# Optimization experiments

Hardware: AMD Instinct MI355X
Metric: run time of the kernel (lower is better)

The kernel has to match this reference:

```python
import jax, jax.numpy as jnp
import numpy as np

B, N, DIM = 4, 2048, 64  # batch, seq_len (== gate out dim), model dim (== dim_head)
H, DH = 8, 64            # heads, dim_head


def setup_inputs() -> dict:
    key = jax.random.key(0)
    ks = jax.random.split(key, 12)
    inner = H * DH
    inp = {
        'q': jax.random.normal(ks[0], (B, N, DIM), jnp.float32),
        'k': jax.random.normal(ks[1], (B, N, DIM), jnp.float32),
        'v': jax.random.normal(ks[2], (B, N, DIM), jnp.float32),
        'Wq': jax.random.normal(ks[3], (inner, DIM), jnp.float32) * 0.05,
        'Wk': jax.random.normal(ks[4], (inner, DIM), jnp.float32) * 0.05,
        'Wv': jax.random.normal(ks[5], (inner, DIM), jnp.float32) * 0.05,
        'Wo': jax.random.normal(ks[6], (DIM, inner), jnp.float32) * 0.05,
        'bo': jax.random.normal(ks[7], (DIM,), jnp.float32) * 0.05,
        'Wg': jax.random.normal(ks[8], (N, DIM), jnp.float32) * 0.05,
        's_local': jnp.float32(1.0),
        's_long': jnp.float32(1.0),
        # recurrent compressive-memory state; positive to avoid 0/0 of zero-init buffers
        'mem': jax.random.uniform(ks[9], (H, DH, DH), jnp.float32) + 0.5,
        'mem_norm': jax.random.uniform(ks[10], (H, N, 1), jnp.float32) + 0.5,
    }
    return inp


def _heads(x, W):
    # x: (B,N,DIM) @ W.T (DIM, H*DH) -> (B,H,N,DH)
    y = x @ W.T
    return y.reshape(x.shape[0], x.shape[1], H, DH).transpose(0, 2, 1, 3)


def reference(q, k, v, Wq, Wk, Wv, Wo, bo, Wg, s_local, s_long, mem, mem_norm):
    scale = DH ** -0.5
    qh, kh, vh = _heads(q, Wq), _heads(k, Wk), _heads(v, Wv)  # (B,H,N,DH)

    # local softmax attention, down-gated by (1 - sigmoid(local scalar))
    sim = jnp.einsum('bhnd,bhmd->bhnm', qh, kh) * scale
    local_attn = jax.nn.softmax(sim, axis=-1) * (1.0 - jax.nn.sigmoid(s_local))

    # query compressive memory: elu(q) @ M / (elu(q) * norm)
    eq = jax.nn.elu(qh)
    mem_q = jnp.einsum('bhnd,hde->bhne', eq, mem) / (eq * mem_norm[None])  # (B,H,N,DH)
    gated = jax.nn.sigmoid(s_long) * jnp.einsum('bhnd,md->bhnm', mem_q, Wg)  # (B,H,N,N)

    attn = local_attn + gated
    out = jnp.einsum('bhnm,bhmd->bhnd', attn, vh)
    out = out.transpose(0, 2, 1, 3).reshape(q.shape[0], q.shape[1], H * DH)
    out = out @ Wo.T + bo  # (B,N,DIM)

    # memory update (state side effect in the original forward)
    ek = jax.nn.elu(kh)
    v_term = vh - jnp.einsum('bhnd,hde->bhne', ek, mem) / (ek * mem_norm[None])
    new_mem = mem[None] + jnp.einsum('bhnd,bhne->bhde', ek, v_term)  # (B,H,DH,DH)
    new_norm = ek.sum(-1)  # (B,H,N)
    return out, new_mem, new_norm
```

## Files before the change

kernel.cpp:

```cpp
#include <hip/hip_runtime.h>
#include <math.h>


#define B_   4
#define N_   2048
#define H_   8
#define BH_  32
#define KP   72

typedef __bf16 bf16x8 __attribute__((ext_vector_type(8)));
typedef __bf16 bf16x4 __attribute__((ext_vector_type(4)));
typedef float  f32x4  __attribute__((ext_vector_type(4)));

__device__ __forceinline__ float eluf(float x) {
    return x > 0.0f ? x : expm1f(x);
}

__global__ __launch_bounds__(256) void k_proj(
    const float* __restrict__ q, const float* __restrict__ k, const float* __restrict__ v,
    const float* __restrict__ Wq, const float* __restrict__ Wk, const float* __restrict__ Wv,
    __bf16* __restrict__ qb, float* __restrict__ kh, __bf16* __restrict__ kb,
    __bf16* __restrict__ vb, __bf16* __restrict__ vbT)
{
    const int which = blockIdx.z;
    const float* __restrict__ src = (which == 0) ? q : (which == 1) ? k : v;
    const float* __restrict__ W   = (which == 0) ? Wq : (which == 1) ? Wk : Wv;
    const int h    = blockIdx.y;
    const int row0 = blockIdx.x * 64;

    __shared__ __align__(16) float AsT[64][68];
    __shared__ __align__(16) float WsT[64][68];
    const int tid = threadIdx.x;
    for (int s = 0; s < 16; ++s) {
        int flat = s * 256 + tid;
        int r = flat >> 6, d = flat & 63;
        AsT[d][r] = src[(size_t)(row0 + r) * 64 + d];
        WsT[d][r] = W[(size_t)(h * 64 + r) * 64 + d];
    }
    __syncthreads();

    const int ty = tid >> 4, tx = tid & 15;
    float acc[4][4];
    #pragma unroll
    for (int i = 0; i < 4; ++i)
        #pragma unroll
        for (int j = 0; j < 4; ++j) acc[i][j] = 0.0f;
    for (int kd = 0; kd < 64; ++kd) {
        float4 a4 = *(const float4*)&AsT[kd][ty * 4];
        float4 w4 = *(const float4*)&WsT[kd][tx * 4];
        float a[4] = {a4.x, a4.y, a4.z, a4.w};
        float w[4] = {w4.x, w4.y, w4.z, w4.w};
        #pragma unroll
        for (int i = 0; i < 4; ++i)
            #pragma unroll
            for (int j = 0; j < 4; ++j) acc[i][j] = fmaf(a[i], w[j], acc[i][j]);
    }

    const int b = row0 >> 11, nb = row0 & 2047;
    if (which == 0) {
        #pragma unroll
        for (int i = 0; i < 4; ++i) {
            size_t idx = ((((size_t)b * H_ + h) * N_ + nb + ty * 4 + i) << 6) + tx * 4;
            bf16x4 o4 = {(__bf16)acc[i][0], (__bf16)acc[i][1],
                         (__bf16)acc[i][2], (__bf16)acc[i][3]};
            *(bf16x4*)&qb[idx] = o4;
        }
    } else if (which == 1) {
        #pragma unroll
        for (int i = 0; i < 4; ++i) {
            size_t idx = ((((size_t)b * H_ + h) * N_ + nb + ty * 4 + i) << 6) + tx * 4;
            *(float4*)&kh[idx] = make_float4(acc[i][0], acc[i][1], acc[i][2], acc[i][3]);
            bf16x4 o4 = {(__bf16)acc[i][0], (__bf16)acc[i][1],
                         (__bf16)acc[i][2], (__bf16)acc[i][3]};
            *(bf16x4*)&kb[idx] = o4;
        }
    } else {
        #pragma unroll
        for (int i = 0; i < 4; ++i) {
            size_t idx = ((((size_t)b * H_ + h) * N_ + nb + ty * 4 + i) << 6) + tx * 4;
            bf16x4 o4 = {(__bf16)acc[i][0], (__bf16)acc[i][1],
                         (__bf16)acc[i][2], (__bf16)acc[i][3]};
            *(bf16x4*)&vb[idx] = o4;
        }
        __syncthreads();
        #pragma unroll
        for (int i = 0; i < 4; ++i)
            #pragma unroll
            for (int j = 0; j < 4; ++j) WsT[tx * 4 + j][ty * 4 + i] = acc[i][j];
        __syncthreads();
        const int e = tid >> 2, nc = (tid & 3) * 16;
        bf16x8 lo, hi;
        #pragma unroll
        for (int jj = 0; jj < 8; ++jj) {
            lo[jj] = (__bf16)WsT[e][nc + jj];
            hi[jj] = (__bf16)WsT[e][nc + 8 + jj];
        }
        size_t base = (((size_t)b * H_ + h) * 64 + e) * (size_t)N_ + nb + nc;
        *(bf16x8*)&vbT[base]     = lo;
        *(bf16x8*)&vbT[base + 8] = hi;
    }
}

__global__ __launch_bounds__(256) void k_memacc(
    const float* __restrict__ kh, const __bf16* __restrict__ vb,
    const float* __restrict__ mem, const float* __restrict__ mem_norm,
    float* __restrict__ pmem, float* __restrict__ out_norm)
{
    const int chunk = blockIdx.x;
    const int bh    = blockIdx.y;
    const int h     = bh & 7;
    const int n0    = chunk * 128;

    __shared__ __align__(16) __bf16 memT_hi[64 * KP], memT_lo[64 * KP];
    __shared__ __align__(16) __bf16 ekn_hi[64 * KP],  ekn_lo[64 * KP];
    __shared__ __align__(16) __bf16 ekT_hi[64 * KP],  ekT_lo[64 * KP];
    __shared__ __align__(16) __bf16 vtT_hi[64 * KP],  vtT_lo[64 * KP];

    const int tid  = threadIdx.x;
    const int w    = tid >> 6, lane = tid & 63;
    const int quad = lane >> 4, m = lane & 15;

    for (int s = 0; s < 16; ++s) {
        int flat = s * 256 + tid;
        int d = flat >> 6, e = flat & 63;
        float mv = mem[(size_t)h * 4096 + flat];
        __bf16 hi = (__bf16)mv;
        memT_hi[e * KP + d] = hi;
        memT_lo[e * KP + d] = (__bf16)(mv - (float)hi);
    }

    f32x4 accM[4];
    #pragma unroll
    for (int t = 0; t < 4; ++t) { f32x4 z = {0.f, 0.f, 0.f, 0.f}; accM[t] = z; }
    __syncthreads();

    for (int sub = 0; sub < 2; ++sub) {
        const int nb = n0 + sub * 64;
        for (int rr = w; rr < 64; rr += 4) {
            const int n = nb + rr;
            float ekv = eluf(kh[((size_t)bh * N_ + n) * 64 + lane]);
            __bf16 hi = (__bf16)ekv;
            __bf16 lo = (__bf16)(ekv - (float)hi);
            ekn_hi[rr * KP + lane] = hi;
            ekn_lo[rr * KP + lane] = lo;
            ekT_hi[lane * KP + rr] = hi;
            ekT_lo[lane * KP + rr] = lo;
            float srt = ekv;
            #pragma unroll
            for (int m2 = 32; m2; m2 >>= 1) srt += __shfl_xor(srt, m2, 64);
            if (lane == 0) out_norm[(size_t)bh * N_ + n] = srt;
        }
        __syncthreads();

        f32x4 km[4];
        #pragma unroll
        for (int t = 0; t < 4; ++t) { f32x4 z = {0.f, 0.f, 0.f, 0.f}; km[t] = z; }
        #pragma unroll
        for (int c2 = 0; c2 < 2; ++c2) {
            bf16x8 Ah = *(const bf16x8*)&ekn_hi[(w * 16 + m) * KP + c2 * 32 + quad * 8];
            bf16x8 Al = *(const bf16x8*)&ekn_lo[(w * 16 + m) * KP + c2 * 32 + quad * 8];
            #pragma unroll
            for (int et = 0; et < 4; ++et) {
                bf16x8 Bh = *(const bf16x8*)&memT_hi[(et * 16 + m) * KP + c2 * 32 + quad * 8];
                bf16x8 Bl = *(const bf16x8*)&memT_lo[(et * 16 + m) * KP + c2 * 32 + quad * 8];
                km[et] = __builtin_amdgcn_mfma_f32_16x16x32_bf16(Al, Bh, km[et], 0, 0, 0);
                km[et] = __builtin_amdgcn_mfma_f32_16x16x32_bf16(Ah, Bl, km[et], 0, 0, 0);
                km[et] = __builtin_amdgcn_mfma_f32_16x16x32_bf16(Ah, Bh, km[et], 0, 0, 0);
            }
        }
        float nrmv[4];
        #pragma unroll
        for (int r = 0; r < 4; ++r)
            nrmv[r] = mem_norm[(size_t)h * N_ + nb + w * 16 + quad * 4 + r];
        #pragma unroll
        for (int et = 0; et < 4; ++et) {
            #pragma unroll
            for (int r = 0; r < 4; ++r) {
                const int nl = w * 16 + quad * 4 + r;
                const int e  = et * 16 + m;
                float vh  = (float)vb[((size_t)bh * N_ + nb + nl) * 64 + e];
                float ekv = (float)ekn_hi[nl * KP + e] + (float)ekn_lo[nl * KP + e];
                float vt  = vh - km[et][r] / (ekv * nrmv[r]);
                __bf16 hi = (__bf16)vt;
                vtT_hi[e * KP + nl] = hi;
                vtT_lo[e * KP + nl] = (__bf16)(vt - (float)hi);
            }
        }
        __syncthreads();

        #pragma unroll
        for (int c2 = 0; c2 < 2; ++c2) {
            bf16x8 Ah = *(const bf16x8*)&ekT_hi[(w * 16 + m) * KP + c2 * 32 + quad * 8];
            bf16x8 Al = *(const bf16x8*)&ekT_lo[(w * 16 + m) * KP + c2 * 32 + quad * 8];
            #pragma unroll
            for (int et = 0; et < 4; ++et) {
                bf16x8 Bh = *(const bf16x8*)&vtT_hi[(et * 16 + m) * KP + c2 * 32 + quad * 8];
                bf16x8 Bl = *(const bf16x8*)&vtT_lo[(et * 16 + m) * KP + c2 * 32 + quad * 8];
                accM[et] = __builtin_amdgcn_mfma_f32_16x16x32_bf16(Al, Bh, accM[et], 0, 0, 0);
                accM[et] = __builtin_amdgcn_mfma_f32_16x16x32_bf16(Ah, Bl, accM[et], 0, 0, 0);
                accM[et] = __builtin_amdgcn_mfma_f32_16x16x32_bf16(Ah, Bh, accM[et], 0, 0, 0);
            }
        }
        __syncthreads();
    }

    const size_t base = ((size_t)chunk * BH_ + bh) * 4096;
    #pragma unroll
    for (int et = 0; et < 4; ++et)
        #pragma unroll
        for (int r = 0; r < 4; ++r)
            pmem[base + (size_t)(w * 16 + quad * 4 + r) * 64 + et * 16 + m] =
                accM[et][r];
}

__global__ __launch_bounds__(256) void k_gv(
    const float* __restrict__ Wg, const __bf16* __restrict__ vbT,
    float* __restrict__ pGv)
{
    const int chunk = blockIdx.x;
    const int bh    = blockIdx.y;
    const int n0    = chunk * 128;
    __shared__ __align__(16) __bf16 WgT[64 * 136];
    const int tid  = threadIdx.x;
    const int w    = tid >> 6, lane = tid & 63;
    const int quad = lane >> 4, m = tid & 15;

    for (int s = 0; s < 8; ++s) {
        int f4 = s * 256 + tid;
        int n = f4 >> 4, dg = (f4 & 15) * 4;
        float4 wv = *(const float4*)&Wg[(size_t)(n0 + n) * 64 + dg];
        WgT[(dg + 0) * 136 + n] = (__bf16)wv.x;
        WgT[(dg + 1) * 136 + n] = (__bf16)wv.y;
        WgT[(dg + 2) * 136 + n] = (__bf16)wv.z;
        WgT[(dg + 3) * 136 + n] = (__bf16)wv.w;
    }
    __syncthreads();

    f32x4 acc[4];
    #pragma unroll
    for (int t = 0; t < 4; ++t) { f32x4 z = {0.f, 0.f, 0.f, 0.f}; acc[t] = z; }
    #pragma unroll
    for (int c = 0; c < 4; ++c) {
        bf16x8 Af = *(const bf16x8*)&WgT[(w * 16 + m) * 136 + c * 32 + quad * 8];
        #pragma unroll
        for (int et = 0; et < 4; ++et) {
            bf16x8 Bf = *(const bf16x8*)&vbT[((size_t)bh * 64 + et * 16 + m) * N_ +
                                             n0 + c * 32 + quad * 8];
            acc[et] = __builtin_amdgcn_mfma_f32_16x16x32_bf16(Af, Bf, acc[et], 0, 0, 0);
        }
    }
    const size_t base = ((size_t)chunk * BH_ + bh) * 4096;
    #pragma unroll
    for (int et = 0; et < 4; ++et)
        #pragma unroll
        for (int r = 0; r < 4; ++r)
            pGv[base + (size_t)(w * 16 + quad * 4 + r) * 64 + et * 16 + m] =
                acc[et][r];
}

__global__ __launch_bounds__(256) void k_reduce(
    const float* __restrict__ mem, const float* __restrict__ pmem,
    const float* __restrict__ pGv, float* __restrict__ out_mem, float* __restrict__ Gv)
{
    const int idx = blockIdx.x * 256 + threadIdx.x;
    const int bh = idx >> 12, h = bh & 7, de = idx & 4095;
    float sm = mem[(size_t)h * 4096 + de];
    float sg = 0.0f;
    #pragma unroll
    for (int c = 0; c < 16; ++c) {
        sm += pmem[(size_t)c * 131072 + idx];
        sg += pGv[(size_t)c * 131072 + idx];
    }
    out_mem[idx] = sm;
    Gv[idx] = sg;
}

__global__ __launch_bounds__(256, 4) void k_flash(
    const __bf16* __restrict__ qb, const __bf16* __restrict__ kb,
    const __bf16* __restrict__ vbT, const float* __restrict__ mem,
    const float* __restrict__ mem_norm, const float* __restrict__ Gv,
    const float* __restrict__ s_local_p, const float* __restrict__ s_long_p,
    __bf16* __restrict__ o)
{
    const int n0 = blockIdx.x * 128;
    const int bh = blockIdx.y;
    const int h  = bh & 7;
    const __bf16* __restrict__ kbp = kb  + (size_t)bh * N_ * 64;
    const __bf16* __restrict__ vtp = vbT + (size_t)bh * 64 * N_;

    __shared__ __align__(16) __bf16 Kb[64 * KP];
    __shared__ __align__(16) __bf16 VT[64 * KP];
    __shared__ __align__(16) __bf16 Pw[128 * KP];
    __shared__ float lsl[128];
    __shared__ float nrm_l[128];

    const int tid  = threadIdx.x;
    const int w    = tid >> 6, lane = tid & 63;
    const int quad = lane >> 4, m = lane & 15;
    const float gl   = 1.0f - 1.0f / (1.0f + __expf(-s_local_p[0]));
    const float sigg = 1.0f / (1.0f + __expf(-s_long_p[0]));

    if (tid < 128) nrm_l[tid] = mem_norm[(size_t)h * N_ + n0 + tid];

    const size_t q0 = ((size_t)bh * N_ + n0 + w * 32 + m) * 64;
    const size_t q1 = q0 + 16 * 64;
    bf16x8 qa00 = *(const bf16x8*)&qb[q0 + quad * 8];
    bf16x8 qa01 = *(const bf16x8*)&qb[q0 + 32 + quad * 8];
    bf16x8 qa10 = *(const bf16x8*)&qb[q1 + quad * 8];
    bf16x8 qa11 = *(const bf16x8*)&qb[q1 + 32 + quad * 8];

    f32x4 O0[4], O1[4];
    #pragma unroll
    for (int t = 0; t < 4; ++t) {
        f32x4 z = {0.f, 0.f, 0.f, 0.f};
        O0[t] = z; O1[t] = z;
    }
    float lsum0 = 0.f, lsum1 = 0.f;
    const int pr0 = w * 32, pr1 = w * 32 + 16;

    const int srow = tid >> 2, scg = (tid & 3) * 16;
    bf16x8 pk0 = *(const bf16x8*)&kbp[(size_t)srow * 64 + scg];
    bf16x8 pk1 = *(const bf16x8*)&kbp[(size_t)srow * 64 + scg + 8];
    bf16x8 pv0 = *(const bf16x8*)&vtp[(size_t)srow * N_ + scg];
    bf16x8 pv1 = *(const bf16x8*)&vtp[(size_t)srow * N_ + scg + 8];

    for (int c = 0; c < 32; ++c) {
        __syncthreads();
        *(bf16x8*)&Kb[srow * KP + scg]     = pk0;
        *(bf16x8*)&Kb[srow * KP + scg + 8] = pk1;
        *(bf16x8*)&VT[srow * KP + scg]     = pv0;
        *(bf16x8*)&VT[srow * KP + scg + 8] = pv1;
        __syncthreads();
        if (c + 1 < 32) {
            const size_t kn = (size_t)((c + 1) * 64 + srow) * 64 + scg;
            const size_t vn = (size_t)srow * N_ + (c + 1) * 64 + scg;
            pk0 = *(const bf16x8*)&kbp[kn];
            pk1 = *(const bf16x8*)&kbp[kn + 8];
            pv0 = *(const bf16x8*)&vtp[vn];
            pv1 = *(const bf16x8*)&vtp[vn + 8];
        }

        f32x4 s0[4], s1[4];
        #pragma unroll
        for (int t = 0; t < 4; ++t) {
            bf16x8 ka0 = *(const bf16x8*)&Kb[(t * 16 + m) * KP + quad * 8];
            bf16x8 ka1 = *(const bf16x8*)&Kb[(t * 16 + m) * KP + 32 + quad * 8];
            f32x4 z = {0.f, 0.f, 0.f, 0.f};
            z = __builtin_amdgcn_mfma_f32_16x16x32_bf16(ka0, qa00, z, 0, 0, 0);
            s0[t] = __builtin_amdgcn_mfma_f32_16x16x32_bf16(ka1, qa01, z, 0, 0, 0);
            f32x4 z2 = {0.f, 0.f, 0.f, 0.f};
            z2 = __builtin_amdgcn_mfma_f32_16x16x32_bf16(ka0, qa10, z2, 0, 0, 0);
            s1[t] = __builtin_amdgcn_mfma_f32_16x16x32_bf16(ka1, qa11, z2, 0, 0, 0);
        }

        #pragma unroll
        for (int t = 0; t < 4; ++t) {
            float p0 = __expf(s0[t][0] * 0.125f), p1 = __expf(s0[t][1] * 0.125f);
            float p2 = __expf(s0[t][2] * 0.125f), p3 = __expf(s0[t][3] * 0.125f);
            lsum0 += p0 + p1 + p2 + p3;
            bf16x4 pk = {(__bf16)p0, (__bf16)p1, (__bf16)p2, (__bf16)p3};
            *(bf16x4*)&Pw[(pr0 + m) * KP + t * 16 + quad * 4] = pk;
            float r0 = __expf(s1[t][0] * 0.125f), r1 = __expf(s1[t][1] * 0.125f);
            float r2 = __expf(s1[t][2] * 0.125f), r3 = __expf(s1[t][3] * 0.125f);
            lsum1 += r0 + r1 + r2 + r3;
            bf16x4 rk = {(__bf16)r0, (__bf16)r1, (__bf16)r2, (__bf16)r3};
            *(bf16x4*)&Pw[(pr1 + m) * KP + t * 16 + quad * 4] = rk;
        }
        asm volatile("s_waitcnt lgkmcnt(0)" ::: "memory");

        #pragma unroll
        for (int c2 = 0; c2 < 2; ++c2) {
            bf16x8 pa0 = *(const bf16x8*)&Pw[(pr0 + m) * KP + c2 * 32 + quad * 8];
            bf16x8 pa1 = *(const bf16x8*)&Pw[(pr1 + m) * KP + c2 * 32 + quad * 8];
            #pragma unroll
            for (int t = 0; t < 4; ++t) {
                bf16x8 vv = *(const bf16x8*)&VT[(t * 16 + m) * KP + c2 * 32 + quad * 8];
                O0[t] = __builtin_amdgcn_mfma_f32_16x16x32_bf16(pa0, vv, O0[t], 0, 0, 0);
                O1[t] = __builtin_amdgcn_mfma_f32_16x16x32_bf16(pa1, vv, O1[t], 0, 0, 0);
            }
        }
    }

    lsum0 += __shfl_xor(lsum0, 16, 64); lsum0 += __shfl_xor(lsum0, 32, 64);
    lsum1 += __shfl_xor(lsum1, 16, 64); lsum1 += __shfl_xor(lsum1, 32, 64);
    if (lane < 16) { lsl[pr0 + lane] = lsum0; lsl[pr1 + lane] = lsum1; }

    __syncthreads();
    for (int s2 = 0; s2 < 16; ++s2) {
        int flat = s2 * 256 + tid;
        int d = flat >> 6, e = flat & 63;
        Kb[e * KP + d] = (__bf16)mem[(size_t)h * 4096 + flat];
        VT[e * KP + d] = (__bf16)Gv[(size_t)bh * 4096 + flat];
    }
    __syncthreads();

    __bf16* op = o + ((size_t)bh * N_ + n0) * 64;
    #pragma unroll
    for (int s = 0; s < 2; ++s) {
        const int prs = w * 32 + s * 16;
        bf16x8 ea0, ea1;
        #pragma unroll
        for (int j = 0; j < 8; ++j) {
            ea0[j] = (__bf16)eluf((float)(s == 0 ? qa00[j] : qa10[j]));
            ea1[j] = (__bf16)eluf((float)(s == 0 ? qa01[j] : qa11[j]));
        }
        f32x4 num[4];
        #pragma unroll
        for (int t = 0; t < 4; ++t) {
            bf16x8 b0 = *(const bf16x8*)&Kb[(t * 16 + m) * KP + quad * 8];
            bf16x8 b1 = *(const bf16x8*)&Kb[(t * 16 + m) * KP + 32 + quad * 8];
            f32x4 z = {0.f, 0.f, 0.f, 0.f};
            z = __builtin_amdgcn_mfma_f32_16x16x32_bf16(ea0, b0, z, 0, 0, 0);
            num[t] = __builtin_amdgcn_mfma_f32_16x16x32_bf16(ea1, b1, z, 0, 0, 0);
        }
        *(bf16x8*)&Pw[(prs + m) * KP + quad * 8]      = ea0;
        *(bf16x8*)&Pw[(prs + m) * KP + 32 + quad * 8] = ea1;
        asm volatile("s_waitcnt lgkmcnt(0)" ::: "memory");
        float mq[4][4];
        #pragma unroll
        for (int t = 0; t < 4; ++t)
            #pragma unroll
            for (int r = 0; r < 4; ++r) {
                float eqv = (float)Pw[(prs + quad * 4 + r) * KP + t * 16 + m];
                mq[t][r] = num[t][r] / (eqv * nrm_l[prs + quad * 4 + r]);
            }
        #pragma unroll
        for (int t = 0; t < 4; ++t)
            #pragma unroll
            for (int r = 0; r < 4; ++r)
                Pw[(prs + quad * 4 + r) * KP + t * 16 + m] = (__bf16)mq[t][r];
        asm volatile("s_waitcnt lgkmcnt(0)" ::: "memory");
        bf16x8 ma0 = *(const bf16x8*)&Pw[(prs + m) * KP + quad * 8];
        bf16x8 ma1 = *(const bf16x8*)&Pw[(prs + m) * KP + 32 + quad * 8];

        #pragma unroll
        for (int t = 0; t < 4; ++t) {
            bf16x8 g0 = *(const bf16x8*)&VT[(t * 16 + m) * KP + quad * 8];
            bf16x8 g1 = *(const bf16x8*)&VT[(t * 16 + m) * KP + 32 + quad * 8];
            f32x4 z = {0.f, 0.f, 0.f, 0.f};
            z = __builtin_amdgcn_mfma_f32_16x16x32_bf16(ma0, g0, z, 0, 0, 0);
            f32x4 o2 = __builtin_amdgcn_mfma_f32_16x16x32_bf16(ma1, g1, z, 0, 0, 0);
            const f32x4 Oc = (s == 0) ? O0[t] : O1[t];
            #pragma unroll
            for (int r = 0; r < 4; ++r) {
                const int qr = prs + quad * 4 + r;
                float val = Oc[r] * (gl / lsl[qr]) + sigg * o2[r];
                op[(size_t)qr * 64 + t * 16 + m] = (__bf16)val;
            }
        }
    }
}

__global__ __launch_bounds__(256) void k_outproj(
    const __bf16* __restrict__ o, const float* __restrict__ Wo,
    const float* __restrict__ bo, float* __restrict__ out)
{
    const int row0 = blockIdx.x * 64;
    const int b = row0 >> 11, nb = row0 & 2047;
    __shared__ __align__(16) __bf16 WoS[64 * 40];
    const int tid  = threadIdx.x;
    const int w    = tid >> 6, lane = tid & 63;
    const int quad = lane >> 4, m = lane & 15;

    f32x4 acc[4];
    #pragma unroll
    for (int t = 0; t < 4; ++t) { f32x4 z = {0.f, 0.f, 0.f, 0.f}; acc[t] = z; }

    for (int kbk = 0; kbk < 16; ++kbk) {
        for (int s2 = 0; s2 < 8; ++s2) {
            int flat = s2 * 256 + tid;
            int n = flat >> 5, kk = flat & 31;
            WoS[n * 40 + kk] = (__bf16)Wo[(size_t)n * 512 + kbk * 32 + kk];
        }
        __syncthreads();
        const int hc = kbk >> 1;
        size_t arow = (((size_t)b * H_ + hc) * N_ + nb + w * 16 + m);
        bf16x8 af = *(const bf16x8*)&o[arow * 64 + (kbk & 1) * 32 + quad * 8];
        #pragma unroll
        for (int t = 0; t < 4; ++t) {
            bf16x8 bf_ = *(const bf16x8*)&WoS[(t * 16 + m) * 40 + quad * 8];
            acc[t] = __builtin_amdgcn_mfma_f32_16x16x32_bf16(af, bf_, acc[t], 0, 0, 0);
        }
        __syncthreads();
    }
    #pragma unroll
    for (int t = 0; t < 4; ++t) {
        float bias = bo[t * 16 + m];
        #pragma unroll
        for (int r = 0; r < 4; ++r)
            out[(size_t)(row0 + w * 16 + quad * 4 + r) * 64 + t * 16 + m] =
                acc[t][r] + bias;
    }
}

extern "C" void kernel_launch(void* const* d_in, const int* in_sizes, int n_in,
                              void* d_out, int out_size, void* d_ws, size_t ws_size,
                              hipStream_t stream)
{
    const float* q        = (const float*)d_in[0];
    const float* k        = (const float*)d_in[1];
    const float* v        = (const float*)d_in[2];
    const float* Wq       = (const float*)d_in[3];
    const float* Wk       = (const float*)d_in[4];
    const float* Wv       = (const float*)d_in[5];
    const float* Wo       = (const float*)d_in[6];
    const float* bo       = (const float*)d_in[7];
    const float* Wg       = (const float*)d_in[8];
    const float* s_local  = (const float*)d_in[9];
    const float* s_long   = (const float*)d_in[10];
    const float* mem      = (const float*)d_in[11];
    const float* mem_norm = (const float*)d_in[12];

    float* ws = (float*)d_ws;
    float*  kh  = ws;
    __bf16* qb  = (__bf16*)(ws + 4194304);
    __bf16* kb  = (__bf16*)(ws + 6291456);
    __bf16* vb  = (__bf16*)(ws + 8388608);
    __bf16* vbT = (__bf16*)(ws + 10485760);
    float*  Gv  = ws + 12582912;
    float*  pm  = ws + 12713984;
    float*  pg  = ws + 14811136;
    __bf16* o   = (__bf16*)(ws + 12713984);

    float* out      = (float*)d_out;
    float* out_mem  = out + 524288;
    float* out_norm = out + 655360;

    k_proj   <<<dim3(128, 8, 3), 256, 0, stream>>>(q, k, v, Wq, Wk, Wv,
                                                   qb, kh, kb, vb, vbT);
    k_memacc <<<dim3(16, 32),    256, 0, stream>>>(kh, vb, mem, mem_norm,
                                                   pm, out_norm);
    k_gv     <<<dim3(16, 32),    256, 0, stream>>>(Wg, vbT, pg);
    k_reduce <<<dim3(512),       256, 0, stream>>>(mem, pm, pg, out_mem, Gv);
    k_flash  <<<dim3(16, 32),    256, 0, stream>>>(qb, kb, vbT, mem, mem_norm, Gv,
                                                   s_local, s_long, o);
    k_outproj<<<dim3(128),       256, 0, stream>>>(o, Wo, bo, out);
}
```

Baseline: 221.7 us.

## Fold softmax scale into K, use MFMA for V projection and norm sums

Several independent tweaks land together. The softmax scale times log2(e) is folded into the bf16 K copy so the attention loop can call exp2f with no per-element multiply. The V projection now runs on bf16 MFMA with an LDS-staged transpose instead of the fp32 FMA path. The elu(k) row sums are computed with an MFMA against a ones vector instead of wavefront shuffles, and a division is replaced by a hardware reciprocal. These trade a little precision (bf16 V projection, approximate rcp) for fewer ALU instructions.

```diff
diff --git a/kernel.cpp b/kernel.cpp
--- a/kernel.cpp
+++ b/kernel.cpp
@@ -7,6 +7,7 @@
 #define H_   8
 #define BH_  32
 #define KP   72
+#define SCLK 0.18033688f
 
 typedef __bf16 bf16x8 __attribute__((ext_vector_type(8)));
 typedef __bf16 bf16x4 __attribute__((ext_vector_type(4)));
@@ -23,14 +24,66 @@
     __bf16* __restrict__ vb, __bf16* __restrict__ vbT)
 {
     const int which = blockIdx.z;
-    const float* __restrict__ src = (which == 0) ? q : (which == 1) ? k : v;
-    const float* __restrict__ W   = (which == 0) ? Wq : (which == 1) ? Wk : Wv;
     const int h    = blockIdx.y;
     const int row0 = blockIdx.x * 64;
-
-    __shared__ __align__(16) float AsT[64][68];
-    __shared__ __align__(16) float WsT[64][68];
-    const int tid = threadIdx.x;
+    const int tid  = threadIdx.x;
+    const int b = row0 >> 11, nb = row0 & 2047;
+
+    __shared__ __align__(16) float  AsT[64][68];
+    __shared__ __align__(16) float  WsT[64][68];
+    __shared__ __align__(16) __bf16 Cs[64 * 72];
+
+    if (which == 2) {
+        const int w = tid >> 6, lane = tid & 63;
+        const int quad = lane >> 4, m = lane & 15;
+        const float* ar = v + (size_t)(row0 + w * 16 + m) * 64;
+        bf16x8 a0, a1;
+        #pragma unroll
+        for (int j = 0; j < 8; ++j) {
+            a0[j] = (__bf16)ar[quad * 8 + j];
+            a1[j] = (__bf16)ar[32 + quad * 8 + j];
+        }
+        f32x4 acc[4];
+        #pragma unroll
+        for (int t = 0; t < 4; ++t) {
+            const float* wr = Wv + (size_t)(h * 64 + t * 16 + m) * 64;
+            bf16x8 b0, b1;
+            #pragma unroll
+            for (int j = 0; j < 8; ++j) {
+                b0[j] = (__bf16)wr[quad * 8 + j];
+                b1[j] = (__bf16)wr[32 + quad * 8 + j];
+            }
+            f32x4 z = {0.f, 0.f, 0.f, 0.f};
+            z = __builtin_amdgcn_mfma_f32_16x16x32_bf16(a0, b0, z, 0, 0, 0);
+            acc[t] = __builtin_amdgcn_mfma_f32_16x16x32_bf16(a1, b1, z, 0, 0, 0);
+        }
+        #pragma unroll
+        for (int t = 0; t < 4; ++t)
+            #pragma unroll
+            for (int r = 0; r < 4; ++r)
+                Cs[(w * 16 + quad * 4 + r) * 72 + t * 16 + m] = (__bf16)acc[t][r];
+        __syncthreads();
+        const int rr = tid >> 2, csg = (tid & 3) * 16;
+        bf16x8 r0 = *(const bf16x8*)&Cs[rr * 72 + csg];
+        bf16x8 r1 = *(const bf16x8*)&Cs[rr * 72 + csg + 8];
+        size_t gb = ((((size_t)b * H_ + h) * N_ + nb + rr) << 6) + csg;
+        *(bf16x8*)&vb[gb]     = r0;
+        *(bf16x8*)&vb[gb + 8] = r1;
+        const int e = tid >> 2, ns = (tid & 3) * 16;
+        bf16x8 t0, t1;
+        #pragma unroll
+        for (int j = 0; j < 8; ++j) {
+            t0[j] = Cs[(ns + j) * 72 + e];
+            t1[j] = Cs[(ns + 8 + j) * 72 + e];
+        }
+        size_t base = (((size_t)b * H_ + h) * 64 + e) * (size_t)N_ + nb + ns;
+        *(bf16x8*)&vbT[base]     = t0;
+        *(bf16x8*)&vbT[base + 8] = t1;
+        return;
+    }
+
+    const float* __restrict__ src = (which == 0) ? q : k;
+    const float* __restrict__ W   = (which == 0) ? Wq : Wk;
     for (int s = 0; s < 16; ++s) {
         int flat = s * 256 + tid;
         int r = flat >> 6, d = flat & 63;
@@ -56,7 +109,6 @@
             for (int j = 0; j < 4; ++j) acc[i][j] = fmaf(a[i], w[j], acc[i][j]);
     }
 
-    const int b = row0 >> 11, nb = row0 & 2047;
     if (which == 0) {
         #pragma unroll
         for (int i = 0; i < 4; ++i) {
@@ -65,39 +117,15 @@
                          (__bf16)acc[i][2], (__bf16)acc[i][3]};
             *(bf16x4*)&qb[idx] = o4;
         }
-    } else if (which == 1) {
+    } else {
         #pragma unroll
         for (int i = 0; i < 4; ++i) {
             size_t idx = ((((size_t)b * H_ + h) * N_ + nb + ty * 4 + i) << 6) + tx * 4;
             *(float4*)&kh[idx] = make_float4(acc[i][0], acc[i][1], acc[i][2], acc[i][3]);
-            bf16x4 o4 = {(__bf16)acc[i][0], (__bf16)acc[i][1],
-                         (__bf16)acc[i][2], (__bf16)acc[i][3]};
+            bf16x4 o4 = {(__bf16)(acc[i][0] * SCLK), (__bf16)(acc[i][1] * SCLK),
+                         (__bf16)(acc[i][2] * SCLK), (__bf16)(acc[i][3] * SCLK)};
             *(bf16x4*)&kb[idx] = o4;
         }
-    } else {
-        #pragma unroll
-        for (int i = 0; i < 4; ++i) {
-            size_t idx = ((((size_t)b * H_ + h) * N_ + nb + ty * 4 + i) << 6) + tx * 4;
-            bf16x4 o4 = {(__bf16)acc[i][0], (__bf16)acc[i][1],
-                         (__bf16)acc[i][2], (__bf16)acc[i][3]};
-            *(bf16x4*)&vb[idx] = o4;
-        }
-        __syncthreads();
-        #pragma unroll
-        for (int i = 0; i < 4; ++i)
-            #pragma unroll
-            for (int j = 0; j < 4; ++j) WsT[tx * 4 + j][ty * 4 + i] = acc[i][j];
-        __syncthreads();
-        const int e = tid >> 2, nc = (tid & 3) * 16;
-        bf16x8 lo, hi;
-        #pragma unroll
-        for (int jj = 0; jj < 8; ++jj) {
-            lo[jj] = (__bf16)WsT[e][nc + jj];
-            hi[jj] = (__bf16)WsT[e][nc + 8 + jj];
-        }
-        size_t base = (((size_t)b * H_ + h) * 64 + e) * (size_t)N_ + nb + nc;
-        *(bf16x8*)&vbT[base]     = lo;
-        *(bf16x8*)&vbT[base + 8] = hi;
     }
 }
 
@@ -128,6 +156,10 @@
         memT_hi[e * KP + d] = hi;
         memT_lo[e * KP + d] = (__bf16)(mv - (float)hi);
     }
+
+    bf16x8 onesv;
+    #pragma unroll
+    for (int j = 0; j < 8; ++j) onesv[j] = (m == 0) ? (__bf16)1.0f : (__bf16)0.0f;
 
     f32x4 accM[4];
     #pragma unroll
@@ -145,20 +177,19 @@
             ekn_lo[rr * KP + lane] = lo;
             ekT_hi[lane * KP + rr] = hi;
             ekT_lo[lane * KP + rr] = lo;
-            float srt = ekv;
-            #pragma unroll
-            for (int m2 = 32; m2; m2 >>= 1) srt += __shfl_xor(srt, m2, 64);
-            if (lane == 0) out_norm[(size_t)bh * N_ + n] = srt;
         }
         __syncthreads();
 
         f32x4 km[4];
         #pragma unroll
         for (int t = 0; t < 4; ++t) { f32x4 z = {0.f, 0.f, 0.f, 0.f}; km[t] = z; }
+        f32x4 nsum = {0.f, 0.f, 0.f, 0.f};
         #pragma unroll
         for (int c2 = 0; c2 < 2; ++c2) {
             bf16x8 Ah = *(const bf16x8*)&ekn_hi[(w * 16 + m) * KP + c2 * 32 + quad * 8];
             bf16x8 Al = *(const bf16x8*)&ekn_lo[(w * 16 + m) * KP + c2 * 32 + quad * 8];
+            nsum = __builtin_amdgcn_mfma_f32_16x16x32_bf16(Ah, onesv, nsum, 0, 0, 0);
+            nsum = __builtin_amdgcn_mfma_f32_16x16x32_bf16(Al, onesv, nsum, 0, 0, 0);
             #pragma unroll
             for (int et = 0; et < 4; ++et) {
                 bf16x8 Bh = *(const bf16x8*)&memT_hi[(et * 16 + m) * KP + c2 * 32 + quad * 8];
@@ -168,6 +199,11 @@
                 km[et] = __builtin_amdgcn_mfma_f32_16x16x32_bf16(Ah, Bh, km[et], 0, 0, 0);
             }
         }
+        if (m == 0) {
+            #pragma unroll
+            for (int r = 0; r < 4; ++r)
+                out_norm[(size_t)bh * N_ + nb + w * 16 + quad * 4 + r] = nsum[r];
+        }
         float nrmv[4];
         #pragma unroll
         for (int r = 0; r < 4; ++r)
@@ -180,7 +216,7 @@
                 const int e  = et * 16 + m;
                 float vh  = (float)vb[((size_t)bh * N_ + nb + nl) * 64 + e];
                 float ekv = (float)ekn_hi[nl * KP + e] + (float)ekn_lo[nl * KP + e];
-                float vt  = vh - km[et][r] / (ekv * nrmv[r]);
+                float vt  = vh - km[et][r] * __builtin_amdgcn_rcpf(ekv * nrmv[r]);
                 __bf16 hi = (__bf16)vt;
                 vtT_hi[e * KP + nl] = hi;
                 vtT_lo[e * KP + nl] = (__bf16)(vt - (float)hi);
@@ -355,13 +391,13 @@
 
         #pragma unroll
         for (int t = 0; t < 4; ++t) {
-            float p0 = __expf(s0[t][0] * 0.125f), p1 = __expf(s0[t][1] * 0.125f);
-            float p2 = __expf(s0[t][2] * 0.125f), p3 = __expf(s0[t][3] * 0.125f);
+            float p0 = exp2f(s0[t][0]), p1 = exp2f(s0[t][1]);
+            float p2 = exp2f(s0[t][2]), p3 = exp2f(s0[t][3]);
             lsum0 += p0 + p1 + p2 + p3;
             bf16x4 pk = {(__bf16)p0, (__bf16)p1, (__bf16)p2, (__bf16)p3};
             *(bf16x4*)&Pw[(pr0 + m) * KP + t * 16 + quad * 4] = pk;
-            float r0 = __expf(s1[t][0] * 0.125f), r1 = __expf(s1[t][1] * 0.125f);
-            float r2 = __expf(s1[t][2] * 0.125f), r3 = __expf(s1[t][3] * 0.125f);
+            float r0 = exp2f(s1[t][0]), r1 = exp2f(s1[t][1]);
+            float r2 = exp2f(s1[t][2]), r3 = exp2f(s1[t][3]);
             lsum1 += r0 + r1 + r2 + r3;
             bf16x4 rk = {(__bf16)r0, (__bf16)r1, (__bf16)r2, (__bf16)r3};
             *(bf16x4*)&Pw[(pr1 + m) * KP + t * 16 + quad * 4] = rk;
@@ -440,11 +476,11 @@
             f32x4 z = {0.f, 0.f, 0.f, 0.f};
             z = __builtin_amdgcn_mfma_f32_16x16x32_bf16(ma0, g0, z, 0, 0, 0);
             f32x4 o2 = __builtin_amdgcn_mfma_f32_16x16x32_bf16(ma1, g1, z, 0, 0, 0);
-            const f32x4 Oc = (s == 0) ? O0[t] : O1[t];
             #pragma unroll
             for (int r = 0; r < 4; ++r) {
                 const int qr = prs + quad * 4 + r;
-                float val = Oc[r] * (gl / lsl[qr]) + sigg * o2[r];
+                float val = ((s == 0) ? O0[t][r] : O1[t][r]) * (gl / lsl[qr])
+                            + sigg * o2[r];
                 op[(size_t)qr * 64 + t * 16 + m] = (__bf16)val;
             }
         }
```

After: 217.4 us. No clear change (-1.9%).
